# Performance work log

Measured on AMD Instinct MI355X. Metric: run time of the kernel, lower is better.

Reference implementation:

```python
import jax, jax.numpy as jnp
import numpy as np

H = 64  # hidden_dim


def _lstm_layer(x_seq, w_ih, w_hh, b_ih, b_hh):
    """Single PyTorch-convention LSTM layer, batch_first input [B,S,F] -> [B,S,H]."""
    B = x_seq.shape[0]
    # precompute input-to-gate projections for all timesteps: [B,S,4H]
    xg = jnp.einsum('bsf,gf->bsg', x_seq, w_ih) + b_ih + b_hh

    def step(carry, xt):
        h, c = carry
        gates = xt + h @ w_hh.T  # [B,4H], gate order i,f,g,o
        i, f, g, o = jnp.split(gates, 4, axis=-1)
        c = jax.nn.sigmoid(f) * c + jax.nn.sigmoid(i) * jnp.tanh(g)
        h = jax.nn.sigmoid(o) * jnp.tanh(c)
        return (h, c), h

    init = (jnp.zeros((B, H), x_seq.dtype), jnp.zeros((B, H), x_seq.dtype))
    (_, _), hs = jax.lax.scan(step, init, jnp.swapaxes(xg, 0, 1))  # [S,B,H]
    return jnp.swapaxes(hs, 0, 1)


def setup_inputs() -> dict:
    key = jax.random.key(0)
    ks = jax.random.split(key, 20)
    s = 0.1  # small init scale to avoid gate saturation
    d = {
        'x': jax.random.normal(ks[0], (4096, 256, 5), jnp.float32),
        'w_ih0': s * jax.random.normal(ks[1], (256, 5), jnp.float32),
        'w_hh0': s * jax.random.normal(ks[2], (256, 64), jnp.float32),
        'b_ih0': s * jax.random.normal(ks[3], (256,), jnp.float32),
        'b_hh0': s * jax.random.normal(ks[4], (256,), jnp.float32),
        'w_ih1': s * jax.random.normal(ks[5], (256, 64), jnp.float32),
        'w_hh1': s * jax.random.normal(ks[6], (256, 64), jnp.float32),
        'b_ih1': s * jax.random.normal(ks[7], (256,), jnp.float32),
        'b_hh1': s * jax.random.normal(ks[8], (256,), jnp.float32),
        'eng_w1': s * jax.random.normal(ks[9], (16, 64), jnp.float32),
        'eng_b1': s * jax.random.normal(ks[10], (16,), jnp.float32),
        'eng_w2': s * jax.random.normal(ks[11], (1, 16), jnp.float32),
        'eng_b2': s * jax.random.normal(ks[12], (1,), jnp.float32),
        'prop_w1': s * jax.random.normal(ks[13], (16, 64), jnp.float32),
        'prop_b1': s * jax.random.normal(ks[14], (16,), jnp.float32),
        'prop_w2': s * jax.random.normal(ks[15], (1, 16), jnp.float32),
        'prop_b2': s * jax.random.normal(ks[16], (1,), jnp.float32),
        'seg_w': s * jax.random.normal(ks[17], (5, 64), jnp.float32),
        'seg_b': s * jax.random.normal(ks[18], (5,), jnp.float32),
    }
    return d


def reference(x, w_ih0, w_hh0, b_ih0, b_hh0, w_ih1, w_hh1, b_ih1, b_hh1,
              eng_w1, eng_b1, eng_w2, eng_b2,
              prop_w1, prop_b1, prop_w2, prop_b2, seg_w, seg_b):
    # 2-layer LSTM (inference: dropout = identity)
    h1 = _lstm_layer(x, w_ih0, w_hh0, b_ih0, b_hh0)   # [B,S,64]
    h2 = _lstm_layer(h1, w_ih1, w_hh1, b_ih1, b_hh1)  # [B,S,64]
    last = h2[:, -1, :]                                # [B,64]

    def mlp_head(w1, b1, w2, b2):
        hdn = jax.nn.relu(last @ w1.T + b1)
        return jax.nn.sigmoid(hdn @ w2.T + b2)[:, 0]   # squeeze(-1)

    engagement = mlp_head(eng_w1, eng_b1, eng_w2, eng_b2)   # [B]
    propensity = mlp_head(prop_w1, prop_b1, prop_w2, prop_b2)  # [B]
    segment_logits = last @ seg_w.T + seg_b                  # [B,5]
    return engagement, propensity, segment_logits
```

## Files before the change

kernel.cpp:

```cpp
#include <hip/hip_runtime.h>

typedef __attribute__((ext_vector_type(8))) short short8_t;
typedef __attribute__((ext_vector_type(4))) float f32x4;

#define SEQ  256
#define HID  64
#define FIN  5
#define BB   16
#define TPB  1024
#define BTOT 4096

#define OFF_W0HI 0
#define OFF_W1HI (64*1024)
#define OFF_W2HI (128*1024)
#define OFF_WX   (192*1024)
#define OFF_B1   (208*1024)

#define NL2E 1.44269504088896f
#if __has_builtin(__builtin_amdgcn_exp2f)
#define EXP2(v) __builtin_amdgcn_exp2f(v)
#else
#define EXP2(v) __expf((v) * 0.6931471805599453f)
#endif

__device__ __forceinline__ float rcp_(float v) { return __builtin_amdgcn_rcpf(v); }
__device__ __forceinline__ unsigned short bf16rtn(float v) {
    unsigned int u = __float_as_uint(v);
    u += 0x7fffu + ((u >> 16) & 1u);
    return (unsigned short)(u >> 16);
}
__device__ __forceinline__ float bf16tof(unsigned short h) {
    return __uint_as_float(((unsigned int)h) << 16);
}
__device__ __forceinline__ float sigf(float v) { return rcp_(1.0f + EXP2(v * -NL2E)); }

__global__ void prep_kernel(const float* __restrict__ wih0, const float* __restrict__ whh0,
                            const float* __restrict__ bih0, const float* __restrict__ bhh0,
                            const float* __restrict__ wih1, const float* __restrict__ whh1,
                            const float* __restrict__ bih1, const float* __restrict__ bhh1,
                            unsigned char* __restrict__ ws) {
    int idx = blockIdx.x * blockDim.x + threadIdx.x;
    if (idx < 3 * 16384) {
        int mat = idx / 16384, e = idx % 16384;
        int tk   = e >> 9;
        int lane = (e >> 3) & 63;
        int i    = e & 7;
        int c = 16 * (tk >> 1) + (lane & 15);
        int k = (tk & 1) * 32 + (lane >> 4) * 8 + i;
        int gate = c & 3;
        int row = gate * 64 + (c >> 2);
        float scale = (gate == 2) ? (-2.0f * NL2E) : -NL2E;
        const float* W = (mat == 0) ? whh0 : (mat == 1) ? whh1 : wih1;
        float v = W[row * HID + k] * scale;
        int bhiOff = (mat == 0) ? OFF_W0HI : (mat == 1) ? OFF_W1HI : OFF_W2HI;
        ((unsigned short*)(ws + bhiOff))[e] = bf16rtn(v);
    } else if (idx < 3 * 16384 + 8192) {
        int e = idx - 3 * 16384;
        int w = e >> 9, r2 = e & 511;
        int lane = r2 >> 3, i = r2 & 7;
        int c = 16 * w + (lane & 15);
        int k = (lane >> 4) * 8 + i;
        int gate = c & 3;
        int row = gate * 64 + (c >> 2);
        float scale = (gate == 2) ? (-2.0f * NL2E) : -NL2E;
        unsigned short outv = 0;
        if (k < 15) {
            float v = wih0[row * FIN + (k % 5)] * scale;
            unsigned int vb = __float_as_uint(v);
            if (k < 10) outv = (unsigned short)(vb >> 16);
            else        outv = bf16rtn(v - __uint_as_float(vb & 0xffff0000u));
        } else if (k == 15 || k == 16) {
            float bv = (bih0[row] + bhh0[row]) * scale;
            unsigned int vb = __float_as_uint(bv);
            if (k == 15) outv = (unsigned short)(vb >> 16);
            else         outv = bf16rtn(bv - __uint_as_float(vb & 0xffff0000u));
        }
        ((unsigned short*)(ws + OFF_WX))[e] = outv;
    }
    if (idx < 256) {
        int gate = idx & 3;
        int row = gate * 64 + (idx >> 2);
        float scale = (gate == 2) ? (-2.0f * NL2E) : -NL2E;
        ((float*)(ws + OFF_B1))[idx] = (bih1[row] + bhh1[row]) * scale;
    }
}

__global__ __launch_bounds__(TPB, 4)
void lstm_fused_kernel(const float* __restrict__ x, const unsigned char* __restrict__ ws,
                       const float* __restrict__ ew1, const float* __restrict__ eb1,
                       const float* __restrict__ ew2, const float* __restrict__ eb2,
                       const float* __restrict__ pw1, const float* __restrict__ pb1,
                       const float* __restrict__ pw2, const float* __restrict__ pb2,
                       const float* __restrict__ sw,  const float* __restrict__ sb,
                       float* __restrict__ out) {
    __shared__ __attribute__((aligned(16))) unsigned short VS0[2][2][64][8];
    __shared__ __attribute__((aligned(16))) unsigned short VS1[2][2][64][8];
    __shared__ __attribute__((aligned(16))) unsigned short XF[4][64][8];
    __shared__ float HS[2][16][17];

    const int tid  = threadIdx.x;
    const int lane = tid & 63;
    const int w    = tid >> 6;
    const int b    = lane & 15;
    const int g    = lane >> 4;
    const int b0g  = blockIdx.x * BB;

    for (int i = tid; i < 2 * 2 * 64 * 8; i += TPB) {
        (&VS0[0][0][0][0])[i] = 0; (&VS1[0][0][0][0])[i] = 0;
    }
    for (int i = tid; i < 4 * 64 * 8; i += TPB) (&XF[0][0][0])[i] = 0;

    short8_t A0[2], A1[2], A2[2], AX;
    #pragma unroll
    for (int ks = 0; ks < 2; ++ks) {
        const int fo = ((w * 2 + ks) * 64 + lane) * 16;
        A0[ks] = *(const short8_t*)(ws + OFF_W0HI + fo);
        A1[ks] = *(const short8_t*)(ws + OFF_W1HI + fo);
        A2[ks] = *(const short8_t*)(ws + OFF_W2HI + fo);
    }
    AX = *(const short8_t*)(ws + OFF_WX + (w * 64 + lane) * 16);
    f32x4 bias1v;
    #pragma unroll
    for (int r = 0; r < 4; ++r)
        bias1v[r] = ((const float*)(ws + OFF_B1))[16 * w + 4 * g + r];

    const int wks = w >> 3, wkg = (w >> 1) & 3, wi = 4 * (w & 1) + g;
    unsigned short* st0 = &VS0[0][wks][wkg * 16 + b][wi];
    unsigned short* st1 = &VS1[0][wks][wkg * 16 + b][wi];

    float c1 = 0.f, c2 = 0.f;

#define PACK_X(SLOT, RL) {                                                          \
    unsigned int u0 = __float_as_uint(bx0), u1 = __float_as_uint(bx1),              \
                 u2 = __float_as_uint(bx2), u3 = __float_as_uint(bx3),              \
                 u4 = __float_as_uint(bx4);                                         \
    unsigned int h0 = u0 >> 16, h1 = u1 >> 16, h2 = u2 >> 16,                       \
                 h3 = u3 >> 16, h4 = u4 >> 16;                                      \
    unsigned int l0 = bf16rtn(bx0 - __uint_as_float(u0 & 0xffff0000u));             \
    unsigned int l1 = bf16rtn(bx1 - __uint_as_float(u1 & 0xffff0000u));             \
    unsigned int l2 = bf16rtn(bx2 - __uint_as_float(u2 & 0xffff0000u));             \
    unsigned int l3 = bf16rtn(bx3 - __uint_as_float(u3 & 0xffff0000u));             \
    unsigned int l4 = bf16rtn(bx4 - __uint_as_float(u4 & 0xffff0000u));             \
    uint4 cc0, cc1;                                                                 \
    cc0.x = h0 | (h1 << 16); cc0.y = h2 | (h3 << 16);                               \
    cc0.z = h4 | (l0 << 16); cc0.w = l1 | (l2 << 16);                               \
    cc1.x = l3 | (l4 << 16); cc1.y = h0 | (h1 << 16);                               \
    cc1.z = h2 | (h3 << 16); cc1.w = h4 | (0x3F80u << 16);                          \
    *(uint4*)&XF[SLOT][0 * 16 + (RL)][0] = cc0;                                     \
    *(uint4*)&XF[SLOT][1 * 16 + (RL)][0] = cc1;                                     \
}

#define GATES(av, cc, hv) {                                                         \
    float e1 = EXP2(av[0]);                                                         \
    float e2 = EXP2(av[1]);                                                         \
    float e3 = EXP2(av[2]);                                                         \
    float e4 = EXP2(av[3]);                                                         \
    float fv = rcp_(1.0f + e2);                                                     \
    float ig = (1.0f - e3) * rcp_((1.0f + e1) * (1.0f + e3));                       \
    cc = fmaf(fv, cc, ig);                                                          \
    float e5 = EXP2(cc * (-2.0f * NL2E));                                           \
    hv = (1.0f - e5) * rcp_((1.0f + e4) * (1.0f + e5));                             \
}

    __syncthreads();
    if (tid < 64) {
        int d = tid >> 4, bb = tid & 15;
        const float* xp_ = x + (size_t)(b0g + bb) * (SEQ * FIN) + d * FIN;
        float bx0 = xp_[0], bx1 = xp_[1], bx2 = xp_[2], bx3 = xp_[3], bx4 = xp_[4];
        PACK_X(d, bb)
        XF[d][2 * 16 + bb][0] = 0x3F80;
    }
    __syncthreads();

    {
        short8_t xf0 = *(const short8_t*)&XF[0][lane][0];
        f32x4 aA = {0.f, 0.f, 0.f, 0.f};
        aA = __builtin_amdgcn_mfma_f32_16x16x32_bf16(AX, xf0, aA, 0, 0, 0);
        float hv;
        GATES(aA, c1, hv)
        st0[1 * 1024] = bf16rtn(hv);
    }

#define ITER(P, R, Q, BEN) {                                                            \
    __syncthreads();                                                                    \
    short8_t h20 = *(const short8_t*)&VS1[P][0][lane][0];                               \
    short8_t h21 = *(const short8_t*)&VS1[P][1][lane][0];                               \
    short8_t h10 = *(const short8_t*)&VS0[P ^ 1][0][lane][0];                           \
    short8_t h11 = *(const short8_t*)&VS0[P ^ 1][1][lane][0];                           \
    short8_t xf  = *(const short8_t*)&XF[((R) + 1) & 3][lane][0];                       \
    float bx0, bx1, bx2, bx3, bx4;                                                      \
    const bool bw_ = (BEN) && (w == ((((Q) & 3) << 2) | (R)));                          \
    if (bw_ && lane < 16) {                                                             \
        const float* xp_ = x + (size_t)(b0g + lane) * (SEQ * FIN)                       \
                             + (4 * (Q) + (R) + 4) * FIN;                               \
        bx0 = xp_[0]; bx1 = xp_[1]; bx2 = xp_[2]; bx3 = xp_[3]; bx4 = xp_[4];           \
    }                                                                                   \
    f32x4 dA = bias1v;                                                                  \
    dA = __builtin_amdgcn_mfma_f32_16x16x32_bf16(A1[0], h20, dA, 0, 0, 0);              \
    dA = __builtin_amdgcn_mfma_f32_16x16x32_bf16(A1[1], h21, dA, 0, 0, 0);              \
    dA = __builtin_amdgcn_mfma_f32_16x16x32_bf16(A2[0], h10, dA, 0, 0, 0);              \
    dA = __builtin_amdgcn_mfma_f32_16x16x32_bf16(A2[1], h11, dA, 0, 0, 0);              \
    f32x4 aA = {0.f, 0.f, 0.f, 0.f};                                                    \
    aA = __builtin_amdgcn_mfma_f32_16x16x32_bf16(AX,    xf,  aA, 0, 0, 0);              \
    aA = __builtin_amdgcn_mfma_f32_16x16x32_bf16(A0[0], h10, aA, 0, 0, 0);              \
    aA = __builtin_amdgcn_mfma_f32_16x16x32_bf16(A0[1], h11, aA, 0, 0, 0);              \
    float hv1, hv0;                                                                     \
    GATES(dA, c2, hv1)                                                                  \
    GATES(aA, c1, hv0)                                                                  \
    unsigned int pk_;                                                                   \
    asm("v_cvt_pk_bf16_f32 %0, %1, %2" : "=v"(pk_) : "v"(hv1), "v"(hv0));               \
    st1[STBUF1 * 1024] = (unsigned short)pk_;                                           \
    st0[STBUF0 * 1024] = (unsigned short)(pk_ >> 16);                                   \
    if (bw_ && lane < 16) { PACK_X((R), lane) }                                         \
}

    for (int q = 0; q < 63; ++q) {
        { const int STBUF1 = 1, STBUF0 = 0; ITER(0, 0, q, 1) }
        { const int STBUF1 = 0, STBUF0 = 1; ITER(1, 1, q, 1) }
        { const int STBUF1 = 1, STBUF0 = 0; ITER(0, 2, q, 1) }
        { const int STBUF1 = 0, STBUF0 = 1; ITER(1, 3, q, 1) }
    }
    { const int STBUF1 = 1, STBUF0 = 0; ITER(0, 0, 63, 0) }
    { const int STBUF1 = 0, STBUF0 = 1; ITER(1, 1, 63, 0) }
    { const int STBUF1 = 1, STBUF0 = 0; ITER(0, 2, 63, 0) }
    { const int STBUF1 = 0, STBUF0 = 1; ITER(1, 3, 63, 0) }
#undef ITER
#undef GATES
#undef PACK_X

    __syncthreads();
    if (tid < 256) {
        int hb_ = tid >> 4, hi_ = tid & 15;
        float ae = eb1[hi_], ap = pb1[hi_];
        for (int j = 0; j < HID; ++j) {
            float h = bf16tof(VS1[0][j >> 5][((j >> 3) & 3) * 16 + hb_][j & 7]);
            ae += h * ew1[hi_ * HID + j];
            ap += h * pw1[hi_ * HID + j];
        }
        HS[0][hb_][hi_] = fmaxf(ae, 0.0f);
        HS[1][hb_][hi_] = fmaxf(ap, 0.0f);
    }
    if (tid >= 256 && tid < 256 + 80) {
        int t2 = tid - 256, sbb = t2 / 5, ss = t2 % 5;
        float a = sb[ss];
        for (int j = 0; j < HID; ++j)
            a += bf16tof(VS1[0][j >> 5][((j >> 3) & 3) * 16 + sbb][j & 7]) * sw[ss * HID + j];
        out[2 * BTOT + (size_t)(b0g + sbb) * 5 + ss] = a;
    }
    __syncthreads();
    if (tid < BB) {
        float eo = eb2[0], po = pb2[0];
        #pragma unroll
        for (int i2 = 0; i2 < 16; ++i2) {
            eo += HS[0][tid][i2] * ew2[i2];
            po += HS[1][tid][i2] * pw2[i2];
        }
        out[b0g + tid]        = sigf(eo);
        out[BTOT + b0g + tid] = sigf(po);
    }
}

extern "C" void kernel_launch(void* const* d_in, const int* in_sizes, int n_in,
                              void* d_out, int out_size, void* d_ws, size_t ws_size,
                              hipStream_t stream) {
    const float* x     = (const float*)d_in[0];
    const float* w_ih0 = (const float*)d_in[1];
    const float* w_hh0 = (const float*)d_in[2];
    const float* b_ih0 = (const float*)d_in[3];
    const float* b_hh0 = (const float*)d_in[4];
    const float* w_ih1 = (const float*)d_in[5];
    const float* w_hh1 = (const float*)d_in[6];
    const float* b_ih1 = (const float*)d_in[7];
    const float* b_hh1 = (const float*)d_in[8];
    const float* ew1 = (const float*)d_in[9];
    const float* eb1 = (const float*)d_in[10];
    const float* ew2 = (const float*)d_in[11];
    const float* eb2 = (const float*)d_in[12];
    const float* pw1 = (const float*)d_in[13];
    const float* pb1 = (const float*)d_in[14];
    const float* pw2 = (const float*)d_in[15];
    const float* pb2 = (const float*)d_in[16];
    const float* sw  = (const float*)d_in[17];
    const float* sb  = (const float*)d_in[18];
    float* out = (float*)d_out;
    unsigned char* ws = (unsigned char*)d_ws;

    hipLaunchKernelGGL(prep_kernel, dim3(224), dim3(256), 0, stream,
                       w_ih0, w_hh0, b_ih0, b_hh0, w_ih1, w_hh1, b_ih1, b_hh1, ws);
    hipLaunchKernelGGL(lstm_fused_kernel, dim3(BTOT / BB), dim3(TPB), 0, stream,
                       x, ws, ew1, eb1, ew2, eb2, pw1, pb1, pw2, pb2, sw, sb, out);
}
```

Before: 194.4 us.

## Specialize waves by LSTM layer instead of computing both layers per wave

Splits the 16 waves into two groups: 8 waves compute layer 0 and 8 compute layer 1, each wave now handling two gate tiles of its layer instead of one tile of both layers. This removes the branch-free duplicated work per wave and lets each group's loads and MFMAs interleave across two independent accumulators. It adds wave divergence by group, which can make per-step timing uneven (layer 1 does 8 MFMAs per wave while layer 0 does 6). The x-prefetch is reassigned to layer-0 waves, and xfc is now read one step ahead.

```diff
diff --git a/kernel.cpp b/kernel.cpp
--- a/kernel.cpp
+++ b/kernel.cpp
@@ -22,6 +22,8 @@
 #else
 #define EXP2(v) __expf((v) * 0.6931471805599453f)
 #endif
+
+#define MFMA(A, B, C) __builtin_amdgcn_mfma_f32_16x16x32_bf16((A), (B), (C), 0, 0, 0)
 
 __device__ __forceinline__ float rcp_(float v) { return __builtin_amdgcn_rcpf(v); }
 __device__ __forceinline__ unsigned short bf16rtn(float v) {
@@ -104,31 +106,49 @@
     const int b    = lane & 15;
     const int g    = lane >> 4;
     const int b0g  = blockIdx.x * BB;
+    const bool isL0 = (w >= 8);
+    const int wt   = w & 7;
 
     for (int i = tid; i < 2 * 2 * 64 * 8; i += TPB) {
         (&VS0[0][0][0][0])[i] = 0; (&VS1[0][0][0][0])[i] = 0;
     }
     for (int i = tid; i < 4 * 64 * 8; i += TPB) (&XF[0][0][0])[i] = 0;
 
-    short8_t A0[2], A1[2], A2[2], AX;
-    #pragma unroll
-    for (int ks = 0; ks < 2; ++ks) {
-        const int fo = ((w * 2 + ks) * 64 + lane) * 16;
-        A0[ks] = *(const short8_t*)(ws + OFF_W0HI + fo);
-        A1[ks] = *(const short8_t*)(ws + OFF_W1HI + fo);
-        A2[ks] = *(const short8_t*)(ws + OFF_W2HI + fo);
-    }
-    AX = *(const short8_t*)(ws + OFF_WX + (w * 64 + lane) * 16);
-    f32x4 bias1v;
-    #pragma unroll
-    for (int r = 0; r < 4; ++r)
-        bias1v[r] = ((const float*)(ws + OFF_B1))[16 * w + 4 * g + r];
-
-    const int wks = w >> 3, wkg = (w >> 1) & 3, wi = 4 * (w & 1) + g;
-    unsigned short* st0 = &VS0[0][wks][wkg * 16 + b][wi];
-    unsigned short* st1 = &VS1[0][wks][wkg * 16 + b][wi];
-
-    float c1 = 0.f, c2 = 0.f;
+    short8_t Fa[2][2], Fb[2][2], FX2[2];
+    f32x4 biasA, biasB;
+    if (!isL0) {
+        #pragma unroll
+        for (int s = 0; s < 2; ++s)
+            #pragma unroll
+            for (int ks = 0; ks < 2; ++ks) {
+                const int fo = (((wt + 8 * s) * 2 + ks) * 64 + lane) * 16;
+                Fa[s][ks] = *(const short8_t*)(ws + OFF_W1HI + fo);
+                Fb[s][ks] = *(const short8_t*)(ws + OFF_W2HI + fo);
+            }
+        #pragma unroll
+        for (int r = 0; r < 4; ++r) {
+            biasA[r] = ((const float*)(ws + OFF_B1))[16 * wt + 4 * g + r];
+            biasB[r] = ((const float*)(ws + OFF_B1))[16 * (wt + 8) + 4 * g + r];
+        }
+    } else {
+        #pragma unroll
+        for (int s = 0; s < 2; ++s) {
+            #pragma unroll
+            for (int ks = 0; ks < 2; ++ks) {
+                const int fo = (((wt + 8 * s) * 2 + ks) * 64 + lane) * 16;
+                Fa[s][ks] = *(const short8_t*)(ws + OFF_W0HI + fo);
+            }
+            FX2[s] = *(const short8_t*)(ws + OFF_WX + ((wt + 8 * s) * 64 + lane) * 16);
+        }
+    }
+
+    const int strow  = ((wt >> 1) & 3) * 16 + b;
+    const int stelem = 4 * (wt & 1) + g;
+    unsigned short* sta = isL0 ? &VS0[0][0][strow][stelem] : &VS1[0][0][strow][stelem];
+    unsigned short* stb = sta + 512;
+
+    float ca = 0.f, cb = 0.f;
+    short8_t xfc;
 
 #define PACK_X(SLOT, RL) {                                                          \
     unsigned int u0 = __float_as_uint(bx0), u1 = __float_as_uint(bx1),              \
@@ -172,58 +192,77 @@
     }
     __syncthreads();
 
-    {
+    if (isL0) {
         short8_t xf0 = *(const short8_t*)&XF[0][lane][0];
-        f32x4 aA = {0.f, 0.f, 0.f, 0.f};
-        aA = __builtin_amdgcn_mfma_f32_16x16x32_bf16(AX, xf0, aA, 0, 0, 0);
-        float hv;
-        GATES(aA, c1, hv)
-        st0[1 * 1024] = bf16rtn(hv);
-    }
-
-#define ITER(P, R, Q, BEN) {                                                            \
+        f32x4 a0 = {0.f, 0.f, 0.f, 0.f}, a1 = {0.f, 0.f, 0.f, 0.f};
+        a0 = MFMA(FX2[0], xf0, a0);
+        a1 = MFMA(FX2[1], xf0, a1);
+        float hva, hvb;
+        GATES(a0, ca, hva)
+        GATES(a1, cb, hvb)
+        unsigned int pk_;
+        asm("v_cvt_pk_bf16_f32 %0, %1, %2" : "=v"(pk_) : "v"(hva), "v"(hvb));
+        sta[1 * 1024] = (unsigned short)pk_;
+        stb[1 * 1024] = (unsigned short)(pk_ >> 16);
+        xfc = *(const short8_t*)&XF[1][lane][0];
+    }
+
+#define ITER(P, R, QEXPR, BEN) {                                                        \
     __syncthreads();                                                                    \
-    short8_t h20 = *(const short8_t*)&VS1[P][0][lane][0];                               \
-    short8_t h21 = *(const short8_t*)&VS1[P][1][lane][0];                               \
-    short8_t h10 = *(const short8_t*)&VS0[P ^ 1][0][lane][0];                           \
-    short8_t h11 = *(const short8_t*)&VS0[P ^ 1][1][lane][0];                           \
-    short8_t xf  = *(const short8_t*)&XF[((R) + 1) & 3][lane][0];                       \
-    float bx0, bx1, bx2, bx3, bx4;                                                      \
-    const bool bw_ = (BEN) && (w == ((((Q) & 3) << 2) | (R)));                          \
-    if (bw_ && lane < 16) {                                                             \
-        const float* xp_ = x + (size_t)(b0g + lane) * (SEQ * FIN)                       \
-                             + (4 * (Q) + (R) + 4) * FIN;                               \
-        bx0 = xp_[0]; bx1 = xp_[1]; bx2 = xp_[2]; bx3 = xp_[3]; bx4 = xp_[4];           \
+    if (!isL0) {                                                                        \
+        short8_t h20 = *(const short8_t*)&VS1[P][0][lane][0];                           \
+        short8_t h21 = *(const short8_t*)&VS1[P][1][lane][0];                           \
+        short8_t h10 = *(const short8_t*)&VS0[P ^ 1][0][lane][0];                       \
+        short8_t h11 = *(const short8_t*)&VS0[P ^ 1][1][lane][0];                       \
+        f32x4 d0 = biasA, d1 = biasB;                                                   \
+        d0 = MFMA(Fa[0][0], h20, d0); d1 = MFMA(Fa[1][0], h20, d1);                     \
+        d0 = MFMA(Fa[0][1], h21, d0); d1 = MFMA(Fa[1][1], h21, d1);                     \
+        d0 = MFMA(Fb[0][0], h10, d0); d1 = MFMA(Fb[1][0], h10, d1);                     \
+        d0 = MFMA(Fb[0][1], h11, d0); d1 = MFMA(Fb[1][1], h11, d1);                     \
+        float hva, hvb;                                                                 \
+        GATES(d0, ca, hva)                                                              \
+        GATES(d1, cb, hvb)                                                              \
+        unsigned int pk_;                                                               \
+        asm("v_cvt_pk_bf16_f32 %0, %1, %2" : "=v"(pk_) : "v"(hva), "v"(hvb));           \
+        sta[(P ^ 1) * 1024] = (unsigned short)pk_;                                      \
+        stb[(P ^ 1) * 1024] = (unsigned short)(pk_ >> 16);                              \
+    } else {                                                                            \
+        const int IDX_ = 4 * (QEXPR) + (R);                                             \
+        const bool bw_ = (BEN) && (w == 8 + (IDX_ & 7));                                \
+        float bx0, bx1, bx2, bx3, bx4;                                                  \
+        if (bw_ && lane < 16) {                                                         \
+            const float* xp_ = x + (size_t)(b0g + lane) * (SEQ * FIN)                   \
+                                 + (IDX_ + 4) * FIN;                                    \
+            bx0 = xp_[0]; bx1 = xp_[1]; bx2 = xp_[2]; bx3 = xp_[3]; bx4 = xp_[4];       \
+        }                                                                               \
+        short8_t h10 = *(const short8_t*)&VS0[P ^ 1][0][lane][0];                       \
+        short8_t h11 = *(const short8_t*)&VS0[P ^ 1][1][lane][0];                       \
+        f32x4 a0 = {0.f, 0.f, 0.f, 0.f}, a1 = {0.f, 0.f, 0.f, 0.f};                     \
+        a0 = MFMA(FX2[0], xfc, a0); a1 = MFMA(FX2[1], xfc, a1);                         \
+        a0 = MFMA(Fa[0][0], h10, a0); a1 = MFMA(Fa[1][0], h10, a1);                     \
+        a0 = MFMA(Fa[0][1], h11, a0); a1 = MFMA(Fa[1][1], h11, a1);                     \
+        float hva, hvb;                                                                 \
+        GATES(a0, ca, hva)                                                              \
+        GATES(a1, cb, hvb)                                                              \
+        unsigned int pk_;                                                               \
+        asm("v_cvt_pk_bf16_f32 %0, %1, %2" : "=v"(pk_) : "v"(hva), "v"(hvb));           \
+        sta[P * 1024] = (unsigned short)pk_;                                            \
+        stb[P * 1024] = (unsigned short)(pk_ >> 16);                                    \
+        if (bw_ && lane < 16) { PACK_X((R), lane) }                                     \
+        xfc = *(const short8_t*)&XF[((R) + 2) & 3][lane][0];                            \
     }                                                                                   \
-    f32x4 dA = bias1v;                                                                  \
-    dA = __builtin_amdgcn_mfma_f32_16x16x32_bf16(A1[0], h20, dA, 0, 0, 0);              \
-    dA = __builtin_amdgcn_mfma_f32_16x16x32_bf16(A1[1], h21, dA, 0, 0, 0);              \
-    dA = __builtin_amdgcn_mfma_f32_16x16x32_bf16(A2[0], h10, dA, 0, 0, 0);              \
-    dA = __builtin_amdgcn_mfma_f32_16x16x32_bf16(A2[1], h11, dA, 0, 0, 0);              \
-    f32x4 aA = {0.f, 0.f, 0.f, 0.f};                                                    \
-    aA = __builtin_amdgcn_mfma_f32_16x16x32_bf16(AX,    xf,  aA, 0, 0, 0);              \
-    aA = __builtin_amdgcn_mfma_f32_16x16x32_bf16(A0[0], h10, aA, 0, 0, 0);              \
-    aA = __builtin_amdgcn_mfma_f32_16x16x32_bf16(A0[1], h11, aA, 0, 0, 0);              \
-    float hv1, hv0;                                                                     \
-    GATES(dA, c2, hv1)                                                                  \
-    GATES(aA, c1, hv0)                                                                  \
-    unsigned int pk_;                                                                   \
-    asm("v_cvt_pk_bf16_f32 %0, %1, %2" : "=v"(pk_) : "v"(hv1), "v"(hv0));               \
-    st1[STBUF1 * 1024] = (unsigned short)pk_;                                           \
-    st0[STBUF0 * 1024] = (unsigned short)(pk_ >> 16);                                   \
-    if (bw_ && lane < 16) { PACK_X((R), lane) }                                         \
 }
 
     for (int q = 0; q < 63; ++q) {
-        { const int STBUF1 = 1, STBUF0 = 0; ITER(0, 0, q, 1) }
-        { const int STBUF1 = 0, STBUF0 = 1; ITER(1, 1, q, 1) }
-        { const int STBUF1 = 1, STBUF0 = 0; ITER(0, 2, q, 1) }
-        { const int STBUF1 = 0, STBUF0 = 1; ITER(1, 3, q, 1) }
-    }
-    { const int STBUF1 = 1, STBUF0 = 0; ITER(0, 0, 63, 0) }
-    { const int STBUF1 = 0, STBUF0 = 1; ITER(1, 1, 63, 0) }
-    { const int STBUF1 = 1, STBUF0 = 0; ITER(0, 2, 63, 0) }
-    { const int STBUF1 = 0, STBUF0 = 1; ITER(1, 3, 63, 0) }
+        ITER(0, 0, q, 1)
+        ITER(1, 1, q, 1)
+        ITER(0, 2, q, 1)
+        ITER(1, 3, q, 1)
+    }
+    ITER(0, 0, 63, 0)
+    ITER(1, 1, 63, 0)
+    ITER(0, 2, 63, 0)
+    ITER(1, 3, 63, 0)
 #undef ITER
 #undef GATES
 #undef PACK_X
```

New measurement: 184.4 us. 1.05x faster.
